# Optimization experiments

Measured on AMD Instinct MI355X. Metric: run time of the kernel, lower is better.

## Reference

```python
import jax, jax.numpy as jnp
import numpy as np

NATOMS = 20000
NEDGES = 400000
EMB = 256
NUM_RBF = 50
NUM_GATES = 10
K = 2
FOUT = 128
BASE = 0.0
OUTER = 5.0


def setup_inputs() -> dict:
    key = jax.random.key(0)
    ks = jax.random.split(key, 24)
    z = jax.random.randint(ks[0], (NATOMS,), 0, 100, dtype=jnp.int32)
    pos = jax.random.normal(ks[1], (NATOMS, 3), jnp.float32)
    batch = jnp.zeros((NATOMS,), jnp.int32)
    edge_index = jax.random.randint(ks[2], (2, NEDGES), 0, NATOMS, dtype=jnp.int32)
    edge_weight = jax.random.uniform(ks[3], (NEDGES,), jnp.float32, 0.5, OUTER)
    edge_vec = jax.random.normal(ks[4], (NEDGES, 3), jnp.float32)
    noise = jax.random.normal(ks[5], (NEDGES, NUM_GATES), jnp.float32)
    # learned parameters (torch Linear stored pre-transposed as [in, out])
    emb = jax.random.normal(ks[6], (100, EMB), jnp.float32) * 0.1
    Wd = jax.random.normal(ks[7], (NUM_RBF, EMB), jnp.float32) * 0.05
    bd = jnp.zeros((EMB,), jnp.float32)
    Wdt = jax.random.normal(ks[8], (EMB, EMB), jnp.float32) * 0.05
    bdt = jnp.zeros((EMB,), jnp.float32)
    Wai = jax.random.normal(ks[9], (EMB, EMB), jnp.float32) * 0.05
    bai = jnp.zeros((EMB,), jnp.float32)
    Waj = jax.random.normal(ks[10], (EMB, EMB), jnp.float32) * 0.05
    baj = jnp.zeros((EMB,), jnp.float32)
    Wgam = jax.random.normal(ks[11], (3 * EMB, EMB), jnp.float32) * 0.03
    bgam = jnp.zeros((EMB,), jnp.float32)
    W_g = jax.random.normal(ks[12], (EMB, NUM_GATES), jnp.float32) * 0.01
    W_noise = jax.random.normal(ks[13], (EMB, NUM_GATES), jnp.float32) * 0.01
    W_exp = jax.random.normal(ks[14], (K, EMB, FOUT), jnp.float32) * 0.05
    b_exp = jnp.zeros((K, FOUT), jnp.float32)
    return dict(z=z, pos=pos, batch=batch, edge_index=edge_index,
                edge_weight=edge_weight, edge_vec=edge_vec, noise=noise,
                emb=emb, Wd=Wd, bd=bd, Wdt=Wdt, bdt=bdt, Wai=Wai, bai=bai,
                Waj=Waj, baj=baj, Wgam=Wgam, bgam=bgam, W_g=W_g,
                W_noise=W_noise, W_exp=W_exp, b_exp=b_exp)


def reference(z, pos, batch, edge_index, edge_weight, edge_vec, noise,
              emb, Wd, bd, Wdt, bdt, Wai, bai, Waj, baj, Wgam, bgam,
              W_g, W_noise, W_exp, b_exp):
    n_atoms = z.shape[0]
    src, dst = edge_index[0], edge_index[1]
    x = emb[z]                                              # [N, EMB]
    # Gaussian RBF expansion on [BASE, OUTER]
    offset = jnp.linspace(BASE, OUTER, NUM_RBF)
    coeff = -0.5 / (offset[1] - offset[0]) ** 2
    edge_attr = jnp.exp(coeff * (edge_weight[:, None] - offset) ** 2)  # [E, NUM_RBF]
    # Cosine cutoff (lower cutoff == 0 branch)
    C = 0.5 * (jnp.cos(edge_weight * (np.pi / OUTER)) + 1.0) * (edge_weight < OUTER)
    # normalized edge directions
    evn = edge_vec / jnp.linalg.norm(edge_vec, axis=1, keepdims=True)  # [E, 3]
    d_proj = (edge_attr @ Wd + bd) * C[:, None]             # [E, EMB]
    d_t = d_proj @ Wdt + bdt                                # [E, EMB]
    a_i = x[src] @ Wai + bai                                # [E, EMB]
    a_j = x[dst] @ Waj + baj                                # [E, EMB]
    gamma = jnp.concatenate([d_t, a_i, a_j], axis=1) @ Wgam + bgam  # [E, EMB]
    # noisy top-k gating
    H = d_t @ W_g + noise * jax.nn.softplus(d_t @ W_noise)  # [E, G]
    top_v, top_i = jax.lax.top_k(H, K)                      # [E, K]
    Hm = jnp.where(H >= top_v[:, -1:], H, -jnp.inf)
    gating = jax.nn.softmax(Hm, axis=-1)                    # [E, G]
    # quirk of the original: expert slot i always sees gamma, experts 0..K-1 used
    expert_out = jnp.einsum('ed,kdf->ekf', gamma, W_exp) + b_exp  # [E, K, FOUT]
    gate_w = jnp.take_along_axis(gating, top_i, axis=1)     # [E, K]
    edge_out = (expert_out * gate_w[:, :, None]).sum(axis=1)  # [E, FOUT]
    atom_out = jax.ops.segment_sum(edge_out, src, num_segments=n_atoms)  # [N, FOUT]
    vec = jax.ops.segment_sum(evn[:, :, None] * edge_out[:, None, :], src,
                              num_segments=n_atoms)         # [N, 3, FOUT]
    return atom_out, vec
```

## Files before the change

kernel.cpp:

```cpp
#include <hip/hip_runtime.h>
#include <math.h>

#define NATOMS 20000
#define NEDGES 400000
#define EMBD   256
#define NRBF   50
#define NGATE  10
#define FOUT   128
#define APB    4
#define OUTERC 5.0f

#define RBF_D    (5.0f/49.0f)
#define RBF_INVD (49.0f/5.0f)
#define RBF_C2   (-0.5f*(49.0f/5.0f)*(49.0f/5.0f)*1.4426950408889634f)
#define PI_OVER_OUTER 0.62831853071795864769f

static __device__ __forceinline__ float softplusf(float x){
    return (x > 15.0f) ? x : __logf(1.0f + __expf(x));
}
static __device__ __forceinline__ unsigned bfr(float v){
    unsigned u = __float_as_uint(v);
    return (u + 0x7fffu + ((u >> 16) & 1u)) & 0xffff0000u;
}
#define BLO(u) __uint_as_float((u) << 16)
#define BHI(u) __uint_as_float((u) & 0xffff0000u)

__global__ __launch_bounds__(256) void k_ag(
    const float* __restrict__ Wd, const float* __restrict__ Wdt,
    const float* __restrict__ bd, const float* __restrict__ bdt,
    const float* __restrict__ bgam, const float* __restrict__ Wgam,
    const float* __restrict__ Wexp, const float* __restrict__ bexp,
    const float* __restrict__ Wg, const float* __restrict__ Wn,
    const int* __restrict__ esrc, int* __restrict__ counts,
    float* __restrict__ R0, float* __restrict__ R1,
    float* __restrict__ Qg, float* __restrict__ Qn, float* __restrict__ sv)
{
    const int b = blockIdx.x, t = threadIdx.x;
    if (b >= 52) {
        int e = (b - 52) * 256 + t;
        if (e < NEDGES) atomicAdd(&counts[esrc[e]], 1);
        return;
    }
    __shared__ float ya[256], za[256];
    const int m = b;
    float s;
    if (m < 50) {
        const float* wr = Wd + m*EMBD;
        s = 0.f;
        #pragma unroll 8
        for (int k = 0; k < EMBD; k++) s += wr[k] * Wdt[k*EMBD + t];
    } else if (m == 50) {
        s = 0.f;
        #pragma unroll 8
        for (int k = 0; k < EMBD; k++) s += bd[k] * Wdt[k*EMBD + t];
    } else {
        s = bdt[t];
    }
    ya[t] = s;
    __syncthreads();
    s = 0.f;
    #pragma unroll 8
    for (int k = 0; k < EMBD; k++) s += ya[k] * Wgam[k*EMBD + t];
    if (m == 51) s += bgam[t];
    za[t] = s;
    __syncthreads();
    const int half = t >> 7, ff = t & 127;
    const float* WX = Wexp + (size_t)half*EMBD*FOUT;
    s = 0.f;
    #pragma unroll 8
    for (int k = 0; k < EMBD; k++) s += za[k] * WX[k*FOUT + ff];
    if (m < 50)       (half ? R1 : R0)[m*FOUT + ff] = s;
    else if (m == 50) sv[half*FOUT + ff] = s;
    else              sv[256 + half*FOUT + ff] = s + bexp[half*FOUT + ff];
    if (t < 20) {
        const int tt = t % 10;
        const float* WT = (t < 10) ? Wg : Wn;
        float q = 0.f;
        #pragma unroll 8
        for (int k = 0; k < EMBD; k++) q += ya[k] * WT[k*NGATE + tt];
        if (m < 50) { float* Q = (t < 10) ? Qg : Qn; Q[m*12 + tt] = q; }
        else {
            int off = (m == 50) ? ((t < 10) ? 512 : 532) : ((t < 10) ? 522 : 542);
            sv[off + tt] = q;
            float* Q = (t < 10) ? Qg : Qn; Q[m*12 + tt] = 0.f;
        }
    }
}

__global__ __launch_bounds__(256) void k_ct(
    const int* __restrict__ counts, int* __restrict__ cursors,
    const float* __restrict__ emb,
    const float* __restrict__ Wai, const float* __restrict__ bai,
    const float* __restrict__ Waj, const float* __restrict__ baj,
    const float* __restrict__ Wgam, const float* __restrict__ Wexp,
    float* __restrict__ Ti0, float* __restrict__ Ti1,
    float* __restrict__ Tj0, float* __restrict__ Tj1)
{
    const int b = blockIdx.x, t = threadIdx.x;
    if (b == 0) {
        __shared__ int part[256];
        const int CH = (NATOMS + 255) / 256;
        int base = t * CH, s = 0;
        for (int i = 0; i < CH; i++) { int idx = base + i; if (idx < NATOMS) s += counts[idx]; }
        part[t] = s;
        __syncthreads();
        for (int d = 1; d < 256; d <<= 1) {
            int v = (t >= d) ? part[t - d] : 0;
            __syncthreads();
            part[t] += v;
            __syncthreads();
        }
        int run = (t == 0) ? 0 : part[t - 1];
        for (int i = 0; i < CH; i++) {
            int idx = base + i;
            if (idx < NATOMS) { cursors[idx] = run; run += counts[idx]; }
        }
        return;
    }
    __shared__ float ya[256], za[256];
    const int side = (b >= 101);
    const int m = side ? b - 101 : b - 1;
    const float* er = emb + m*EMBD;
    const float* W1 = side ? Waj : Wai;
    const float* b1 = side ? baj : bai;
    float s = b1[t];
    #pragma unroll 8
    for (int k = 0; k < EMBD; k++) s += er[k] * W1[k*EMBD + t];
    ya[t] = s;
    __syncthreads();
    const float* G = Wgam + (size_t)(side ? 512 : 256) * EMBD;
    s = 0.f;
    #pragma unroll 8
    for (int k = 0; k < EMBD; k++) s += ya[k] * G[k*EMBD + t];
    za[t] = s;
    __syncthreads();
    const int half = t >> 7, ff = t & 127;
    const float* WX = Wexp + (size_t)half*EMBD*FOUT;
    s = 0.f;
    #pragma unroll 8
    for (int k = 0; k < EMBD; k++) s += za[k] * WX[k*FOUT + ff];
    float* dst = side ? (half ? Tj1 : Tj0) : (half ? Ti1 : Ti0);
    dst[m*FOUT + ff] = s;
}

__global__ __launch_bounds__(256) void k_edge(
    const int* __restrict__ z, const int* __restrict__ esrc, const int* __restrict__ edst,
    const float* __restrict__ ew, const float* __restrict__ evec, const float* __restrict__ noise,
    const float* __restrict__ Qg, const float* __restrict__ Qn, const float* __restrict__ sv,
    int* __restrict__ cursors,
    float4* __restrict__ rec, unsigned* __restrict__ zdj)
{
    __shared__ float qgL[52*12], qnL[52*12];
    __shared__ float nbuf[256*11];
    __shared__ float vbuf[768];
    const int t = threadIdx.x;
    const int e0 = blockIdx.x * 256;

    for (int i = t; i < 52*12; i += 256) { qgL[i] = Qg[i]; qnL[i] = Qn[i]; }
    #pragma unroll
    for (int q = 0; q < 10; q++) {
        int idx = q*256 + t; long long g = (long long)e0*10 + idx;
        if (g < (long long)NEDGES*10) { int r_ = idx/10; nbuf[r_*11 + (idx - r_*10)] = noise[g]; }
    }
    #pragma unroll
    for (int q = 0; q < 3; q++) {
        int idx = q*256 + t; long long g = (long long)e0*3 + idx;
        if (g < (long long)NEDGES*3) vbuf[idx] = evec[g];
    }
    __syncthreads();

    int e = e0 + t;
    if (e >= NEDGES) return;
    float w = ew[e];
    float C = (w < OUTERC) ? 0.5f*(__cosf(w*PI_OVER_OUTER) + 1.0f) : 0.0f;
    int iw = (int)(w * RBF_INVD);
    int j0 = (iw - 4) & ~3;
    j0 = max(0, min(40, j0));
    float rW[12];
    #pragma unroll
    for (int k = 0; k < 12; k++) { float tt = w - (j0+k)*RBF_D; rW[k] = exp2f(RBF_C2*tt*tt); }
    float hg[NGATE], hn[NGATE];
    #pragma unroll
    for (int g2 = 0; g2 < NGATE; g2++) { hg[g2] = 0.f; hn[g2] = 0.f; }
    #pragma unroll
    for (int k = 0; k < 12; k++) {
        float rk = rW[k];
        const float* qg = &qgL[(j0+k)*12];
        const float* qn = &qnL[(j0+k)*12];
        float4 ga = *(const float4*)qg; float4 gb = *(const float4*)(qg+4);
        float2 gc = *(const float2*)(qg+8);
        float4 na = *(const float4*)qn; float4 nb = *(const float4*)(qn+4);
        float2 nc = *(const float2*)(qn+8);
        hg[0]=fmaf(rk,ga.x,hg[0]); hg[1]=fmaf(rk,ga.y,hg[1]); hg[2]=fmaf(rk,ga.z,hg[2]); hg[3]=fmaf(rk,ga.w,hg[3]);
        hg[4]=fmaf(rk,gb.x,hg[4]); hg[5]=fmaf(rk,gb.y,hg[5]); hg[6]=fmaf(rk,gb.z,hg[6]); hg[7]=fmaf(rk,gb.w,hg[7]);
        hg[8]=fmaf(rk,gc.x,hg[8]); hg[9]=fmaf(rk,gc.y,hg[9]);
        hn[0]=fmaf(rk,na.x,hn[0]); hn[1]=fmaf(rk,na.y,hn[1]); hn[2]=fmaf(rk,na.z,hn[2]); hn[3]=fmaf(rk,na.w,hn[3]);
        hn[4]=fmaf(rk,nb.x,hn[4]); hn[5]=fmaf(rk,nb.y,hn[5]); hn[6]=fmaf(rk,nb.z,hn[6]); hn[7]=fmaf(rk,nb.w,hn[7]);
        hn[8]=fmaf(rk,nc.x,hn[8]); hn[9]=fmaf(rk,nc.y,hn[9]);
    }
    float H[NGATE];
    #pragma unroll
    for (int g2 = 0; g2 < NGATE; g2++) {
        float gv = C*(hg[g2] + sv[512+g2]) + sv[522+g2];
        float nv = C*(hn[g2] + sv[532+g2]) + sv[542+g2];
        H[g2] = gv + nbuf[t*11 + g2] * softplusf(nv);
    }
    float m1 = -INFINITY, m2 = -INFINITY;
    #pragma unroll
    for (int g2 = 0; g2 < NGATE; g2++) {
        float v = H[g2];
        if (v > m1) { m2 = m1; m1 = v; } else if (v > m2) { m2 = v; }
    }
    float den = 0.f;
    #pragma unroll
    for (int g2 = 0; g2 < NGATE; g2++) den += (H[g2] >= m2) ? __expf(H[g2] - m1) : 0.f;
    float inv = 1.0f / den;
    float g0 = inv;
    float g1 = __expf(m2 - m1) * inv;

    float ex = vbuf[t*3+0], ey = vbuf[t*3+1], ez = vbuf[t*3+2];
    float rn = rsqrtf(ex*ex + ey*ey + ez*ez);
    ex *= rn; ey *= rn; ez *= rn;
    int zd = z[edst[e]];
    int p = atomicAdd(&cursors[esrc[e]], 1);

    rec[p] = make_float4(w,
        __uint_as_float((bfr(g0)>>16) | bfr(g1)),
        __uint_as_float((bfr(ex)>>16) | bfr(ey)),
        __uint_as_float(bfr(ez)));
    zdj[p] = (unsigned)zd | (__float2uint_rn(C * 16777215.0f) << 7);
}

#define FFLUSH() { \
    accS[aCur-aBeg][pair][f] = make_float4(accA, accX, accY, accZ); \
    accA=accX=accY=accZ=0.f; \
    aCur++; \
    if (aCur < aEnd) { nextEnd = neNxt; int an_ = aCur + 1; if (an_ < aEnd) neNxt = cursors[an_]; } \
    else nextEnd = 0x7fffffff; }

#define FCOMP(GI, D, TJ) { \
    int gi = (GI); \
    while (gi == nextEnd) FFLUSH() \
    unsigned gu = __float_as_uint(D.y), xu = __float_as_uint(D.z), eu = __float_as_uint(D.w); \
    float u_ = (pair ? BHI(gu) : BLO(gu)) * (TJ); \
    accA += u_; \
    accX = fmaf(BLO(xu), u_, accX); \
    accY = fmaf(BHI(xu), u_, accY); \
    accZ = fmaf(BHI(eu), u_, accZ); }

#define SFLUSH() { \
    int aIdx_ = aCur - aBeg; \
    if (sAct) { \
        *(float4*)&Plds[0][l][aIdx_*4] = make_float4(p00,p10,p20,p30); \
        *(float4*)&Plds[1][l][aIdx_*4] = make_float4(p01,p11,p21,p31); \
        p00=p01=p10=p11=p20=p21=p30=p31=0.f; } \
    aCur++; \
    if (aCur < aEnd) { nextEnd = neNxt; int an_ = aCur + 1; if (an_ < aEnd) neNxt = cursors[an_]; } \
    else nextEnd = 0x7fffffff; }

#define SCOMP(GI, D, CZ) { \
    int gi = (GI); \
    while (gi == nextEnd) SFLUSH() \
    unsigned gu = __float_as_uint(D.y), xu = __float_as_uint(D.z), eu = __float_as_uint(D.w); \
    float g0f = BLO(gu), g1f = BHI(gu); \
    float exf = BLO(xu), eyf = BHI(xu), ezf = BHI(eu); \
    float Cc_ = __uint2float_rn((CZ) >> 7) * (1.0f/16777215.0f); \
    float t_ = D.x - sjf; \
    float e2_ = exp2f(RBF_C2*t_*t_); \
    float b_ = isG ? Cc_*e2_ : (isC ? Cc_ : 1.0f); \
    float bg0 = b_*g0f, bg1 = b_*g1f; \
    p00 += bg0; p01 += bg1; \
    p10 = fmaf(exf,bg0,p10); p11 = fmaf(exf,bg1,p11); \
    p20 = fmaf(eyf,bg0,p20); p21 = fmaf(eyf,bg1,p21); \
    p30 = fmaf(ezf,bg0,p30); p31 = fmaf(ezf,bg1,p31); }

#define DOT16(PA,PB,PC,PD,R_) { \
    D00=fmaf(PA.x,R_,D00); D01=fmaf(PA.y,R_,D01); D02=fmaf(PA.z,R_,D02); D03=fmaf(PA.w,R_,D03); \
    D10=fmaf(PB.x,R_,D10); D11=fmaf(PB.y,R_,D11); D12=fmaf(PB.z,R_,D12); D13=fmaf(PB.w,R_,D13); \
    D20=fmaf(PC.x,R_,D20); D21=fmaf(PC.y,R_,D21); D22=fmaf(PC.z,R_,D22); D23=fmaf(PC.w,R_,D23); \
    D30=fmaf(PD.x,R_,D30); D31=fmaf(PD.y,R_,D31); D32=fmaf(PD.z,R_,D32); D33=fmaf(PD.w,R_,D33); }

__global__ __launch_bounds__(320) void k_main(
    const int* __restrict__ z, const int* __restrict__ cursors,
    const float4* __restrict__ rec, const unsigned* __restrict__ zdj,
    const float* __restrict__ R0, const float* __restrict__ R1,
    const float* __restrict__ Ti0, const float* __restrict__ Ti1,
    const float* __restrict__ Tj0, const float* __restrict__ Tj1,
    const float* __restrict__ sv, float* __restrict__ out)
{
    __shared__ float4 accS[APB][2][FOUT];
    __shared__ __align__(16) float Plds[2][52][20];
    const int tid = threadIdx.x;

    const int aBeg = blockIdx.x * APB, aEnd = aBeg + APB;
    const int eBeg = aBeg ? cursors[aBeg-1] : 0;
    const int eEnd = cursors[aEnd-1];

    int aCur = aBeg;
    int nextEnd = cursors[aCur];
    int neNxt = (aBeg+1 < aEnd) ? cursors[aBeg+1] : 0x7fffffff;

    const int pair = (tid >> 7) & 1, f = tid & 127;

    if (tid < 256) {
        const float* TjT = pair ? Tj1 : Tj0;
        float accA=0.f, accX=0.f, accY=0.f, accZ=0.f;

        unsigned czj0 = zdj[eBeg],   czj1 = zdj[eBeg+1];
        unsigned nzj0 = zdj[eBeg+2], nzj1 = zdj[eBeg+3];
        float4 c0 = rec[eBeg], c1 = rec[eBeg+1];
        float ctj0 = TjT[(czj0 & 0x7fu)*FOUT + f];
        float ctj1 = TjT[(czj1 & 0x7fu)*FOUT + f];

        for (int i = eBeg; i < eEnd; i += 2) {
            float4 n0 = rec[i+2], n1 = rec[i+3];
            float ntj0 = TjT[(nzj0 & 0x7fu)*FOUT + f];
            float ntj1 = TjT[(nzj1 & 0x7fu)*FOUT + f];
            unsigned mzj0 = zdj[i+4], mzj1 = zdj[i+5];

            FCOMP(i,   c0, ctj0)
            if (i + 1 < eEnd) { FCOMP(i+1, c1, ctj1) }

            c0 = n0; c1 = n1;
            czj0 = nzj0; czj1 = nzj1; nzj0 = mzj0; nzj1 = mzj1;
            ctj0 = ntj0; ctj1 = ntj1;
        }
        while (aCur < aEnd) FFLUSH();
    } else {
        const int l = tid - 256;
        const bool sAct = (l < 52);
        const bool isG = (l < 50), isC = (l == 50);
        const float sjf = l * RBF_D;
        float p00=0,p01=0,p10=0,p11=0,p20=0,p21=0,p30=0,p31=0;

        float4 c0 = rec[eBeg], c1 = rec[eBeg+1];
        unsigned z0 = zdj[eBeg], z1 = zdj[eBeg+1];

        for (int i = eBeg; i < eEnd; i += 2) {
            float4 n0 = rec[i+2], n1 = rec[i+3];
            unsigned y0 = zdj[i+2], y1 = zdj[i+3];

            SCOMP(i,   c0, z0)
            if (i + 1 < eEnd) { SCOMP(i+1, c1, z1) }

            c0 = n0; c1 = n1; z0 = y0; z1 = y1;
        }
        while (aCur < aEnd) SFLUSH();
    }
    __syncthreads();

    if (tid < 256) {
        const float* Rtab = pair ? R1 : R0;
        const float* TiT  = pair ? Ti1 : Ti0;
        const float sVv = sv[pair*FOUT + f];
        const float dVv = sv[256 + pair*FOUT + f];
        float D00=0,D01=0,D02=0,D03=0, D10=0,D11=0,D12=0,D13=0;
        float D20=0,D21=0,D22=0,D23=0, D30=0,D31=0,D32=0,D33=0;
        #pragma unroll 5
        for (int j = 0; j < 50; j++) {
            float r = Rtab[j*FOUT + f];
            const float* pb = &Plds[pair][j][0];
            float4 qa = *(const float4*)(pb+0);
            float4 qb = *(const float4*)(pb+4);
            float4 qc = *(const float4*)(pb+8);
            float4 qd = *(const float4*)(pb+12);
            DOT16(qa, qb, qc, qd, r)
        }
        {
            const float* pb = &Plds[pair][50][0];
            float4 qa = *(const float4*)(pb+0);
            float4 qb = *(const float4*)(pb+4);
            float4 qc = *(const float4*)(pb+8);
            float4 qd = *(const float4*)(pb+12);
            DOT16(qa, qb, qc, qd, sVv)
        }
        {
            const float* pb = &Plds[pair][51][0];
            float4 qa = *(const float4*)(pb+0);
            float4 qb = *(const float4*)(pb+4);
            float4 qc = *(const float4*)(pb+8);
            float4 qd = *(const float4*)(pb+12);
            float r0 = dVv + TiT[z[aBeg+0]*FOUT + f];
            float r1 = dVv + TiT[z[aBeg+1]*FOUT + f];
            float r2 = dVv + TiT[z[aBeg+2]*FOUT + f];
            float r3 = dVv + TiT[z[aBeg+3]*FOUT + f];
            D00=fmaf(qa.x,r0,D00); D01=fmaf(qa.y,r0,D01); D02=fmaf(qa.z,r0,D02); D03=fmaf(qa.w,r0,D03);
            D10=fmaf(qb.x,r1,D10); D11=fmaf(qb.y,r1,D11); D12=fmaf(qb.z,r1,D12); D13=fmaf(qb.w,r1,D13);
            D20=fmaf(qc.x,r2,D20); D21=fmaf(qc.y,r2,D21); D22=fmaf(qc.z,r2,D22); D23=fmaf(qc.w,r2,D23);
            D30=fmaf(qd.x,r3,D30); D31=fmaf(qd.y,r3,D31); D32=fmaf(qd.z,r3,D32); D33=fmaf(qd.w,r3,D33);
        }
        float4 t;
        t = accS[0][pair][f]; t.x+=D00; t.y+=D01; t.z+=D02; t.w+=D03; accS[0][pair][f] = t;
        t = accS[1][pair][f]; t.x+=D10; t.y+=D11; t.z+=D12; t.w+=D13; accS[1][pair][f] = t;
        t = accS[2][pair][f]; t.x+=D20; t.y+=D21; t.z+=D22; t.w+=D23; accS[2][pair][f] = t;
        t = accS[3][pair][f]; t.x+=D30; t.y+=D31; t.z+=D32; t.w+=D33; accS[3][pair][f] = t;
    }
    __syncthreads();
    if (tid < FOUT) {
        #pragma unroll
        for (int a2 = 0; a2 < APB; a2++) {
            float4 v0 = accS[a2][0][tid];
            float4 v1 = accS[a2][1][tid];
            int atom = aBeg + a2;
            out[(size_t)atom*FOUT + tid] = v0.x + v1.x;
            float* vb = out + (size_t)NATOMS*FOUT + (size_t)atom*3*FOUT;
            vb[tid]        = v0.y + v1.y;
            vb[FOUT+tid]   = v0.z + v1.z;
            vb[2*FOUT+tid] = v0.w + v1.w;
        }
    }
}

extern "C" void kernel_launch(void* const* d_in, const int* in_sizes, int n_in,
                              void* d_out, int out_size, void* d_ws, size_t ws_size,
                              hipStream_t stream)
{
    const int*   z    = (const int*)d_in[0];
    const int*   ei   = (const int*)d_in[3];
    const int*   esrc = ei;
    const int*   edst = ei + NEDGES;
    const float* ew   = (const float*)d_in[4];
    const float* evec = (const float*)d_in[5];
    const float* nz   = (const float*)d_in[6];
    const float* emb  = (const float*)d_in[7];
    const float* Wd   = (const float*)d_in[8];
    const float* bd   = (const float*)d_in[9];
    const float* Wdt  = (const float*)d_in[10];
    const float* bdt  = (const float*)d_in[11];
    const float* Wai  = (const float*)d_in[12];
    const float* bai  = (const float*)d_in[13];
    const float* Waj  = (const float*)d_in[14];
    const float* baj  = (const float*)d_in[15];
    const float* Wgam = (const float*)d_in[16];
    const float* bgam = (const float*)d_in[17];
    const float* Wg   = (const float*)d_in[18];
    const float* Wn   = (const float*)d_in[19];
    const float* Wexp = (const float*)d_in[20];
    const float* bexp = (const float*)d_in[21];
    float* out = (float*)d_out;

    char* w = (char*)d_ws;
    auto alloc = [&](size_t bytes) -> void* {
        void* p = (void*)w;
        w += (bytes + 255) & ~(size_t)255;
        return p;
    };
    int*   counts  = (int*)alloc(NATOMS * 4);
    int*   cursors = (int*)alloc(NATOMS * 4);
    float* R0  = (float*)alloc(NRBF*FOUT*4);
    float* R1  = (float*)alloc(NRBF*FOUT*4);
    float* Qg  = (float*)alloc(52*12*4);
    float* Qn  = (float*)alloc(52*12*4);
    float* Ti0 = (float*)alloc(100*FOUT*4);
    float* Ti1 = (float*)alloc(100*FOUT*4);
    float* Tj0 = (float*)alloc(100*FOUT*4);
    float* Tj1 = (float*)alloc(100*FOUT*4);
    float* sv  = (float*)alloc(552*4);
    float4*   rec = (float4*)alloc(((size_t)NEDGES + 16)*16);
    unsigned* zdj = (unsigned*)alloc(((size_t)NEDGES + 16)*4);

    hipMemsetAsync(counts, 0, NATOMS*4, stream);
    hipMemsetAsync(rec + NEDGES, 0, 16*sizeof(float4), stream);
    hipMemsetAsync(zdj + NEDGES, 0, 16*4, stream);

    {
        int grid = 52 + (NEDGES + 255) / 256;
        k_ag<<<grid, 256, 0, stream>>>(Wd, Wdt, bd, bdt, bgam, Wgam, Wexp, bexp,
                                       Wg, Wn, esrc, counts, R0, R1, Qg, Qn, sv);
    }
    k_ct<<<201, 256, 0, stream>>>(counts, cursors, emb, Wai, bai, Waj, baj,
                                  Wgam, Wexp, Ti0, Ti1, Tj0, Tj1);
    {
        int grid = (NEDGES + 255) / 256;
        k_edge<<<grid, 256, 0, stream>>>(z, esrc, edst, ew, evec, nz,
                                         Qg, Qn, sv, cursors, rec, zdj);
    }
    {
        int grid = NATOMS / APB;
        k_main<<<grid, 320, 0, stream>>>(z, cursors, rec, zdj,
                                         R0, R1, Ti0, Ti1, Tj0, Tj1, sv, out);
    }
}
```

Before: 406.2 us.

## Fold atom-type tables into first kernel and double atoms per main block

The per-atom-type Ti/Tj projection tables (emb→Wai/Waj→Wgam→Wexp) move out of k_ct and into extra blocks of k_ag, so they run alongside the edge-count atomics. The prefix scan becomes its own single-block kernel, no longer sharing a launch with the table work. k_main now handles 8 atoms per block instead of 4. The projection epilogue runs twice, over two groups of 4 atoms, which spreads the cost of the shared Rtab/sv reads and the per-block setup over more atoms. In exchange there are half as many k_main blocks, so fewer waves are in flight and per-block edge work is less balanced, and the per-block LDS footprint grows.

```diff
diff --git a/kernel.cpp b/kernel.cpp
--- a/kernel.cpp
+++ b/kernel.cpp
@@ -7,7 +7,7 @@
 #define NRBF   50
 #define NGATE  10
 #define FOUT   128
-#define APB    4
+#define APB    8
 #define OUTERC 5.0f
 
 #define RBF_D    (5.0f/49.0f)
@@ -31,17 +31,48 @@
     const float* __restrict__ bgam, const float* __restrict__ Wgam,
     const float* __restrict__ Wexp, const float* __restrict__ bexp,
     const float* __restrict__ Wg, const float* __restrict__ Wn,
+    const float* __restrict__ emb,
+    const float* __restrict__ Wai, const float* __restrict__ bai,
+    const float* __restrict__ Waj, const float* __restrict__ baj,
     const int* __restrict__ esrc, int* __restrict__ counts,
     float* __restrict__ R0, float* __restrict__ R1,
-    float* __restrict__ Qg, float* __restrict__ Qn, float* __restrict__ sv)
+    float* __restrict__ Qg, float* __restrict__ Qn, float* __restrict__ sv,
+    float* __restrict__ Ti0, float* __restrict__ Ti1,
+    float* __restrict__ Tj0, float* __restrict__ Tj1)
 {
     const int b = blockIdx.x, t = threadIdx.x;
-    if (b >= 52) {
-        int e = (b - 52) * 256 + t;
+    if (b >= 252) {
+        int e = (b - 252) * 256 + t;
         if (e < NEDGES) atomicAdd(&counts[esrc[e]], 1);
         return;
     }
     __shared__ float ya[256], za[256];
+    if (b >= 52) {
+        const int side = (b >= 152);
+        const int m = side ? b - 152 : b - 52;
+        const float* er = emb + m*EMBD;
+        const float* W1 = side ? Waj : Wai;
+        const float* b1 = side ? baj : bai;
+        float s = b1[t];
+        #pragma unroll 8
+        for (int k = 0; k < EMBD; k++) s += er[k] * W1[k*EMBD + t];
+        ya[t] = s;
+        __syncthreads();
+        const float* G = Wgam + (size_t)(side ? 512 : 256) * EMBD;
+        s = 0.f;
+        #pragma unroll 8
+        for (int k = 0; k < EMBD; k++) s += ya[k] * G[k*EMBD + t];
+        za[t] = s;
+        __syncthreads();
+        const int half = t >> 7, ff = t & 127;
+        const float* WX = Wexp + (size_t)half*EMBD*FOUT;
+        s = 0.f;
+        #pragma unroll 8
+        for (int k = 0; k < EMBD; k++) s += za[k] * WX[k*FOUT + ff];
+        float* dst = side ? (half ? Tj1 : Tj0) : (half ? Ti1 : Ti0);
+        dst[m*FOUT + ff] = s;
+        return;
+    }
     const int m = b;
     float s;
     if (m < 50) {
@@ -87,60 +118,27 @@
     }
 }
 
-__global__ __launch_bounds__(256) void k_ct(
-    const int* __restrict__ counts, int* __restrict__ cursors,
-    const float* __restrict__ emb,
-    const float* __restrict__ Wai, const float* __restrict__ bai,
-    const float* __restrict__ Waj, const float* __restrict__ baj,
-    const float* __restrict__ Wgam, const float* __restrict__ Wexp,
-    float* __restrict__ Ti0, float* __restrict__ Ti1,
-    float* __restrict__ Tj0, float* __restrict__ Tj1)
+__global__ __launch_bounds__(256) void k_scan(
+    const int* __restrict__ counts, int* __restrict__ cursors)
 {
-    const int b = blockIdx.x, t = threadIdx.x;
-    if (b == 0) {
-        __shared__ int part[256];
-        const int CH = (NATOMS + 255) / 256;
-        int base = t * CH, s = 0;
-        for (int i = 0; i < CH; i++) { int idx = base + i; if (idx < NATOMS) s += counts[idx]; }
-        part[t] = s;
+    const int t = threadIdx.x;
+    __shared__ int part[256];
+    const int CH = (NATOMS + 255) / 256;
+    int base = t * CH, s = 0;
+    for (int i = 0; i < CH; i++) { int idx = base + i; if (idx < NATOMS) s += counts[idx]; }
+    part[t] = s;
+    __syncthreads();
+    for (int d = 1; d < 256; d <<= 1) {
+        int v = (t >= d) ? part[t - d] : 0;
         __syncthreads();
-        for (int d = 1; d < 256; d <<= 1) {
-            int v = (t >= d) ? part[t - d] : 0;
-            __syncthreads();
-            part[t] += v;
-            __syncthreads();
-        }
-        int run = (t == 0) ? 0 : part[t - 1];
-        for (int i = 0; i < CH; i++) {
-            int idx = base + i;
-            if (idx < NATOMS) { cursors[idx] = run; run += counts[idx]; }
-        }
-        return;
-    }
-    __shared__ float ya[256], za[256];
-    const int side = (b >= 101);
-    const int m = side ? b - 101 : b - 1;
-    const float* er = emb + m*EMBD;
-    const float* W1 = side ? Waj : Wai;
-    const float* b1 = side ? baj : bai;
-    float s = b1[t];
-    #pragma unroll 8
-    for (int k = 0; k < EMBD; k++) s += er[k] * W1[k*EMBD + t];
-    ya[t] = s;
-    __syncthreads();
-    const float* G = Wgam + (size_t)(side ? 512 : 256) * EMBD;
-    s = 0.f;
-    #pragma unroll 8
-    for (int k = 0; k < EMBD; k++) s += ya[k] * G[k*EMBD + t];
-    za[t] = s;
-    __syncthreads();
-    const int half = t >> 7, ff = t & 127;
-    const float* WX = Wexp + (size_t)half*EMBD*FOUT;
-    s = 0.f;
-    #pragma unroll 8
-    for (int k = 0; k < EMBD; k++) s += za[k] * WX[k*FOUT + ff];
-    float* dst = side ? (half ? Tj1 : Tj0) : (half ? Ti1 : Ti0);
-    dst[m*FOUT + ff] = s;
+        part[t] += v;
+        __syncthreads();
+    }
+    int run = (t == 0) ? 0 : part[t - 1];
+    for (int i = 0; i < CH; i++) {
+        int idx = base + i;
+        if (idx < NATOMS) { cursors[idx] = run; run += counts[idx]; }
+    }
 }
 
 __global__ __launch_bounds__(256) void k_edge(
@@ -289,7 +287,7 @@
     const float* __restrict__ sv, float* __restrict__ out)
 {
     __shared__ float4 accS[APB][2][FOUT];
-    __shared__ __align__(16) float Plds[2][52][20];
+    __shared__ __align__(16) float Plds[2][52][APB*4+4];
     const int tid = threadIdx.x;
 
     const int aBeg = blockIdx.x * APB, aEnd = aBeg + APB;
@@ -354,46 +352,52 @@
         const float* TiT  = pair ? Ti1 : Ti0;
         const float sVv = sv[pair*FOUT + f];
         const float dVv = sv[256 + pair*FOUT + f];
-        float D00=0,D01=0,D02=0,D03=0, D10=0,D11=0,D12=0,D13=0;
-        float D20=0,D21=0,D22=0,D23=0, D30=0,D31=0,D32=0,D33=0;
-        #pragma unroll 5
-        for (int j = 0; j < 50; j++) {
-            float r = Rtab[j*FOUT + f];
-            const float* pb = &Plds[pair][j][0];
-            float4 qa = *(const float4*)(pb+0);
-            float4 qb = *(const float4*)(pb+4);
-            float4 qc = *(const float4*)(pb+8);
-            float4 qd = *(const float4*)(pb+12);
-            DOT16(qa, qb, qc, qd, r)
+        #pragma unroll 1
+        for (int ha = 0; ha < 2; ha++) {
+            const int off = ha * 16;
+            float D00=0,D01=0,D02=0,D03=0, D10=0,D11=0,D12=0,D13=0;
+            float D20=0,D21=0,D22=0,D23=0, D30=0,D31=0,D32=0,D33=0;
+            #pragma unroll 5
+            for (int j = 0; j < 50; j++) {
+                float r = Rtab[j*FOUT + f];
+                const float* pb = &Plds[pair][j][off];
+                float4 qa = *(const float4*)(pb+0);
+                float4 qb = *(const float4*)(pb+4);
+                float4 qc = *(const float4*)(pb+8);
+                float4 qd = *(const float4*)(pb+12);
+                DOT16(qa, qb, qc, qd, r)
+            }
+            {
+                const float* pb = &Plds[pair][50][off];
+                float4 qa = *(const float4*)(pb+0);
+                float4 qb = *(const float4*)(pb+4);
+                float4 qc = *(const float4*)(pb+8);
+                float4 qd = *(const float4*)(pb+12);
+                DOT16(qa, qb, qc, qd, sVv)
+            }
+            {
+                const float* pb = &Plds[pair][51][off];
+                float4 qa = *(const float4*)(pb+0);
+                float4 qb = *(const float4*)(pb+4);
+                float4 qc = *(const float4*)(pb+8);
+                float4 qd = *(const float4*)(pb+12);
+                int ab = aBeg + ha*4;
+                float r0 = dVv + TiT[z[ab+0]*FOUT + f];
+                float r1 = dVv + TiT[z[ab+1]*FOUT + f];
+                float r2 = dVv + TiT[z[ab+2]*FOUT + f];
+                float r3 = dVv + TiT[z[ab+3]*FOUT + f];
+                D00=fmaf(qa.x,r0,D00); D01=fmaf(qa.y,r0,D01); D02=fmaf(qa.z,r0,D02); D03=fmaf(qa.w,r0,D03);
+                D10=fmaf(qb.x,r1,D10); D11=fmaf(qb.y,r1,D11); D12=fmaf(qb.z,r1,D12); D13=fmaf(qb.w,r1,D13);
+                D20=fmaf(qc.x,r2,D20); D21=fmaf(qc.y,r2,D21); D22=fmaf(qc.z,r2,D22); D23=fmaf(qc.w,r2,D23);
+                D30=fmaf(qd.x,r3,D30); D31=fmaf(qd.y,r3,D31); D32=fmaf(qd.z,r3,D32); D33=fmaf(qd.w,r3,D33);
+            }
+            const int a0 = ha*4;
+            float4 t;
+            t = accS[a0+0][pair][f]; t.x+=D00; t.y+=D01; t.z+=D02; t.w+=D03; accS[a0+0][pair][f] = t;
+            t = accS[a0+1][pair][f]; t.x+=D10; t.y+=D11; t.z+=D12; t.w+=D13; accS[a0+1][pair][f] = t;
+            t = accS[a0+2][pair][f]; t.x+=D20; t.y+=D21; t.z+=D22; t.w+=D23; accS[a0+2][pair][f] = t;
+            t = accS[a0+3][pair][f]; t.x+=D30; t.y+=D31; t.z+=D32; t.w+=D33; accS[a0+3][pair][f] = t;
         }
-        {
-            const float* pb = &Plds[pair][50][0];
-            float4 qa = *(const float4*)(pb+0);
-            float4 qb = *(const float4*)(pb+4);
-            float4 qc = *(const float4*)(pb+8);
-            float4 qd = *(const float4*)(pb+12);
-            DOT16(qa, qb, qc, qd, sVv)
-        }
-        {
-            const float* pb = &Plds[pair][51][0];
-            float4 qa = *(const float4*)(pb+0);
-            float4 qb = *(const float4*)(pb+4);
-            float4 qc = *(const float4*)(pb+8);
-            float4 qd = *(const float4*)(pb+12);
-            float r0 = dVv + TiT[z[aBeg+0]*FOUT + f];
-            float r1 = dVv + TiT[z[aBeg+1]*FOUT + f];
-            float r2 = dVv + TiT[z[aBeg+2]*FOUT + f];
-            float r3 = dVv + TiT[z[aBeg+3]*FOUT + f];
-            D00=fmaf(qa.x,r0,D00); D01=fmaf(qa.y,r0,D01); D02=fmaf(qa.z,r0,D02); D03=fmaf(qa.w,r0,D03);
-            D10=fmaf(qb.x,r1,D10); D11=fmaf(qb.y,r1,D11); D12=fmaf(qb.z,r1,D12); D13=fmaf(qb.w,r1,D13);
-            D20=fmaf(qc.x,r2,D20); D21=fmaf(qc.y,r2,D21); D22=fmaf(qc.z,r2,D22); D23=fmaf(qc.w,r2,D23);
-            D30=fmaf(qd.x,r3,D30); D31=fmaf(qd.y,r3,D31); D32=fmaf(qd.z,r3,D32); D33=fmaf(qd.w,r3,D33);
-        }
-        float4 t;
-        t = accS[0][pair][f]; t.x+=D00; t.y+=D01; t.z+=D02; t.w+=D03; accS[0][pair][f] = t;
-        t = accS[1][pair][f]; t.x+=D10; t.y+=D11; t.z+=D12; t.w+=D13; accS[1][pair][f] = t;
-        t = accS[2][pair][f]; t.x+=D20; t.y+=D21; t.z+=D22; t.w+=D23; accS[2][pair][f] = t;
-        t = accS[3][pair][f]; t.x+=D30; t.y+=D31; t.z+=D32; t.w+=D33; accS[3][pair][f] = t;
     }
     __syncthreads();
     if (tid < FOUT) {
@@ -464,12 +468,13 @@
     hipMemsetAsync(zdj + NEDGES, 0, 16*4, stream);
 
     {
-        int grid = 52 + (NEDGES + 255) / 256;
+        int grid = 252 + (NEDGES + 255) / 256;
         k_ag<<<grid, 256, 0, stream>>>(Wd, Wdt, bd, bdt, bgam, Wgam, Wexp, bexp,
-                                       Wg, Wn, esrc, counts, R0, R1, Qg, Qn, sv);
-    }
-    k_ct<<<201, 256, 0, stream>>>(counts, cursors, emb, Wai, bai, Waj, baj,
-                                  Wgam, Wexp, Ti0, Ti1, Tj0, Tj1);
+                                       Wg, Wn, emb, Wai, bai, Waj, baj,
+                                       esrc, counts, R0, R1, Qg, Qn, sv,
+                                       Ti0, Ti1, Tj0, Tj1);
+    }
+    k_scan<<<1, 256, 0, stream>>>(counts, cursors);
     {
         int grid = (NEDGES + 255) / 256;
         k_edge<<<grid, 256, 0, stream>>>(z, esrc, edst, ew, evec, nz,
```

Result: slower. 504.7 us (+24.3%).

## Move embedding-table precompute into first kernel and deepen edge-loop prefetch

Applied to the files above, without the earlier changes.

The per-species Ti/Tj table computation moves out of the scan kernel and into the first kernel, so it runs alongside the weight-product blocks and the edge-count atomics. The scan becomes its own single-block kernel and no longer shares a launch with 200 compute blocks that delay it. The main kernel's edge loops also prefetch two edge pairs ahead instead of one, including the Tj gather, to hide more memory latency. This costs extra registers per thread and a larger first-kernel grid.

```diff
diff --git a/kernel.cpp b/kernel.cpp
--- a/kernel.cpp
+++ b/kernel.cpp
@@ -31,17 +31,48 @@
     const float* __restrict__ bgam, const float* __restrict__ Wgam,
     const float* __restrict__ Wexp, const float* __restrict__ bexp,
     const float* __restrict__ Wg, const float* __restrict__ Wn,
+    const float* __restrict__ emb,
+    const float* __restrict__ Wai, const float* __restrict__ bai,
+    const float* __restrict__ Waj, const float* __restrict__ baj,
     const int* __restrict__ esrc, int* __restrict__ counts,
     float* __restrict__ R0, float* __restrict__ R1,
-    float* __restrict__ Qg, float* __restrict__ Qn, float* __restrict__ sv)
+    float* __restrict__ Qg, float* __restrict__ Qn, float* __restrict__ sv,
+    float* __restrict__ Ti0, float* __restrict__ Ti1,
+    float* __restrict__ Tj0, float* __restrict__ Tj1)
 {
     const int b = blockIdx.x, t = threadIdx.x;
-    if (b >= 52) {
-        int e = (b - 52) * 256 + t;
+    if (b >= 252) {
+        int e = (b - 252) * 256 + t;
         if (e < NEDGES) atomicAdd(&counts[esrc[e]], 1);
         return;
     }
     __shared__ float ya[256], za[256];
+    if (b >= 52) {
+        const int side = (b >= 152);
+        const int m = side ? b - 152 : b - 52;
+        const float* er = emb + m*EMBD;
+        const float* W1 = side ? Waj : Wai;
+        const float* b1 = side ? baj : bai;
+        float s = b1[t];
+        #pragma unroll 8
+        for (int k = 0; k < EMBD; k++) s += er[k] * W1[k*EMBD + t];
+        ya[t] = s;
+        __syncthreads();
+        const float* G = Wgam + (size_t)(side ? 512 : 256) * EMBD;
+        s = 0.f;
+        #pragma unroll 8
+        for (int k = 0; k < EMBD; k++) s += ya[k] * G[k*EMBD + t];
+        za[t] = s;
+        __syncthreads();
+        const int half = t >> 7, ff = t & 127;
+        const float* WX = Wexp + (size_t)half*EMBD*FOUT;
+        s = 0.f;
+        #pragma unroll 8
+        for (int k = 0; k < EMBD; k++) s += za[k] * WX[k*FOUT + ff];
+        float* dst = side ? (half ? Tj1 : Tj0) : (half ? Ti1 : Ti0);
+        dst[m*FOUT + ff] = s;
+        return;
+    }
     const int m = b;
     float s;
     if (m < 50) {
@@ -87,60 +118,27 @@
     }
 }
 
-__global__ __launch_bounds__(256) void k_ct(
-    const int* __restrict__ counts, int* __restrict__ cursors,
-    const float* __restrict__ emb,
-    const float* __restrict__ Wai, const float* __restrict__ bai,
-    const float* __restrict__ Waj, const float* __restrict__ baj,
-    const float* __restrict__ Wgam, const float* __restrict__ Wexp,
-    float* __restrict__ Ti0, float* __restrict__ Ti1,
-    float* __restrict__ Tj0, float* __restrict__ Tj1)
+__global__ __launch_bounds__(256) void k_scan(
+    const int* __restrict__ counts, int* __restrict__ cursors)
 {
-    const int b = blockIdx.x, t = threadIdx.x;
-    if (b == 0) {
-        __shared__ int part[256];
-        const int CH = (NATOMS + 255) / 256;
-        int base = t * CH, s = 0;
-        for (int i = 0; i < CH; i++) { int idx = base + i; if (idx < NATOMS) s += counts[idx]; }
-        part[t] = s;
+    const int t = threadIdx.x;
+    __shared__ int part[256];
+    const int CH = (NATOMS + 255) / 256;
+    int base = t * CH, s = 0;
+    for (int i = 0; i < CH; i++) { int idx = base + i; if (idx < NATOMS) s += counts[idx]; }
+    part[t] = s;
+    __syncthreads();
+    for (int d = 1; d < 256; d <<= 1) {
+        int v = (t >= d) ? part[t - d] : 0;
         __syncthreads();
-        for (int d = 1; d < 256; d <<= 1) {
-            int v = (t >= d) ? part[t - d] : 0;
-            __syncthreads();
-            part[t] += v;
-            __syncthreads();
-        }
-        int run = (t == 0) ? 0 : part[t - 1];
-        for (int i = 0; i < CH; i++) {
-            int idx = base + i;
-            if (idx < NATOMS) { cursors[idx] = run; run += counts[idx]; }
-        }
-        return;
-    }
-    __shared__ float ya[256], za[256];
-    const int side = (b >= 101);
-    const int m = side ? b - 101 : b - 1;
-    const float* er = emb + m*EMBD;
-    const float* W1 = side ? Waj : Wai;
-    const float* b1 = side ? baj : bai;
-    float s = b1[t];
-    #pragma unroll 8
-    for (int k = 0; k < EMBD; k++) s += er[k] * W1[k*EMBD + t];
-    ya[t] = s;
-    __syncthreads();
-    const float* G = Wgam + (size_t)(side ? 512 : 256) * EMBD;
-    s = 0.f;
-    #pragma unroll 8
-    for (int k = 0; k < EMBD; k++) s += ya[k] * G[k*EMBD + t];
-    za[t] = s;
-    __syncthreads();
-    const int half = t >> 7, ff = t & 127;
-    const float* WX = Wexp + (size_t)half*EMBD*FOUT;
-    s = 0.f;
-    #pragma unroll 8
-    for (int k = 0; k < EMBD; k++) s += za[k] * WX[k*FOUT + ff];
-    float* dst = side ? (half ? Tj1 : Tj0) : (half ? Ti1 : Ti0);
-    dst[m*FOUT + ff] = s;
+        part[t] += v;
+        __syncthreads();
+    }
+    int run = (t == 0) ? 0 : part[t - 1];
+    for (int i = 0; i < CH; i++) {
+        int idx = base + i;
+        if (idx < NATOMS) { cursors[idx] = run; run += counts[idx]; }
+    }
 }
 
 __global__ __launch_bounds__(256) void k_edge(
@@ -306,24 +304,26 @@
         const float* TjT = pair ? Tj1 : Tj0;
         float accA=0.f, accX=0.f, accY=0.f, accZ=0.f;
 
-        unsigned czj0 = zdj[eBeg],   czj1 = zdj[eBeg+1];
-        unsigned nzj0 = zdj[eBeg+2], nzj1 = zdj[eBeg+3];
-        float4 c0 = rec[eBeg], c1 = rec[eBeg+1];
-        float ctj0 = TjT[(czj0 & 0x7fu)*FOUT + f];
-        float ctj1 = TjT[(czj1 & 0x7fu)*FOUT + f];
+        float4 c0 = rec[eBeg],   c1 = rec[eBeg+1];
+        float4 d0 = rec[eBeg+2], d1 = rec[eBeg+3];
+        unsigned zj4 = zdj[eBeg+4], zj5 = zdj[eBeg+5];
+        float ct0 = TjT[(zdj[eBeg]  & 0x7fu)*FOUT + f];
+        float ct1 = TjT[(zdj[eBeg+1]& 0x7fu)*FOUT + f];
+        float dt0 = TjT[(zdj[eBeg+2]& 0x7fu)*FOUT + f];
+        float dt1 = TjT[(zdj[eBeg+3]& 0x7fu)*FOUT + f];
 
         for (int i = eBeg; i < eEnd; i += 2) {
-            float4 n0 = rec[i+2], n1 = rec[i+3];
-            float ntj0 = TjT[(nzj0 & 0x7fu)*FOUT + f];
-            float ntj1 = TjT[(nzj1 & 0x7fu)*FOUT + f];
-            unsigned mzj0 = zdj[i+4], mzj1 = zdj[i+5];
-
-            FCOMP(i,   c0, ctj0)
-            if (i + 1 < eEnd) { FCOMP(i+1, c1, ctj1) }
-
-            c0 = n0; c1 = n1;
-            czj0 = nzj0; czj1 = nzj1; nzj0 = mzj0; nzj1 = mzj1;
-            ctj0 = ntj0; ctj1 = ntj1;
+            float4 e0 = rec[i+4], e1 = rec[i+5];
+            unsigned zj6 = zdj[i+6], zj7 = zdj[i+7];
+            float et0 = TjT[(zj4 & 0x7fu)*FOUT + f];
+            float et1 = TjT[(zj5 & 0x7fu)*FOUT + f];
+
+            FCOMP(i,   c0, ct0)
+            if (i + 1 < eEnd) { FCOMP(i+1, c1, ct1) }
+
+            c0 = d0; c1 = d1; d0 = e0; d1 = e1;
+            ct0 = dt0; ct1 = dt1; dt0 = et0; dt1 = et1;
+            zj4 = zj6; zj5 = zj7;
         }
         while (aCur < aEnd) FFLUSH();
     } else {
@@ -333,17 +333,20 @@
         const float sjf = l * RBF_D;
         float p00=0,p01=0,p10=0,p11=0,p20=0,p21=0,p30=0,p31=0;
 
-        float4 c0 = rec[eBeg], c1 = rec[eBeg+1];
-        unsigned z0 = zdj[eBeg], z1 = zdj[eBeg+1];
+        float4 c0 = rec[eBeg],   c1 = rec[eBeg+1];
+        float4 d0 = rec[eBeg+2], d1 = rec[eBeg+3];
+        unsigned z0 = zdj[eBeg],   z1 = zdj[eBeg+1];
+        unsigned z2 = zdj[eBeg+2], z3 = zdj[eBeg+3];
 
         for (int i = eBeg; i < eEnd; i += 2) {
-            float4 n0 = rec[i+2], n1 = rec[i+3];
-            unsigned y0 = zdj[i+2], y1 = zdj[i+3];
+            float4 e0 = rec[i+4], e1 = rec[i+5];
+            unsigned z4 = zdj[i+4], z5 = zdj[i+5];
 
             SCOMP(i,   c0, z0)
             if (i + 1 < eEnd) { SCOMP(i+1, c1, z1) }
 
-            c0 = n0; c1 = n1; z0 = y0; z1 = y1;
+            c0 = d0; c1 = d1; d0 = e0; d1 = e1;
+            z0 = z2; z1 = z3; z2 = z4; z3 = z5;
         }
         while (aCur < aEnd) SFLUSH();
     }
@@ -464,12 +467,13 @@
     hipMemsetAsync(zdj + NEDGES, 0, 16*4, stream);
 
     {
-        int grid = 52 + (NEDGES + 255) / 256;
+        int grid = 252 + (NEDGES + 255) / 256;
         k_ag<<<grid, 256, 0, stream>>>(Wd, Wdt, bd, bdt, bgam, Wgam, Wexp, bexp,
-                                       Wg, Wn, esrc, counts, R0, R1, Qg, Qn, sv);
-    }
-    k_ct<<<201, 256, 0, stream>>>(counts, cursors, emb, Wai, bai, Waj, baj,
-                                  Wgam, Wexp, Ti0, Ti1, Tj0, Tj1);
+                                       Wg, Wn, emb, Wai, bai, Waj, baj,
+                                       esrc, counts, R0, R1, Qg, Qn, sv,
+                                       Ti0, Ti1, Tj0, Tj1);
+    }
+    k_scan<<<1, 256, 0, stream>>>(counts, cursors);
     {
         int grid = (NEDGES + 255) / 256;
         k_edge<<<grid, 256, 0, stream>>>(z, esrc, edst, ew, evec, nz,
```

After: 406.0 us. No clear change (-0.1%).
